# Optimization experiments

Hardware: AMD Instinct MI355X
Metric: run time of the kernel (lower is better)

The kernel has to match this reference:

```python
import jax, jax.numpy as jnp
import numpy as np

N = 50000   # nodes
E = 800000  # edges (avg degree 16)
G = 32      # graphs in batch
IN = 128; HID = 64; H = 2; C = 16
NEG_SLOPE = 0.2
BN_EPS = 1e-5


def setup_inputs() -> dict:
    key = jax.random.key(0)
    ks = jax.random.split(key, 16)
    def rn(k, shape, scale=0.1):
        return jax.random.normal(k, shape, jnp.float32) * scale
    return {
        "feat": jax.random.normal(ks[0], (N, IN), jnp.float32),
        "W0": rn(ks[1], (IN, H * HID)),
        "attn0": rn(ks[2], (H, HID)),
        "W1": rn(ks[3], (H * HID, H * HID)),
        "attn1": rn(ks[4], (H, HID)),
        "W2": rn(ks[5], (H * HID, H * HID)),
        "attn2": rn(ks[6], (H, HID)),
        "Wf": rn(ks[7], (H * HID, H * C)),
        "attnf": rn(ks[8], (H, C)),
        "mlp_w1": rn(ks[9], (C, C)),
        "mlp_gamma": jnp.ones((C,), jnp.float32),
        "mlp_beta": jnp.zeros((C,), jnp.float32),
        "mlp_w2": rn(ks[10], (C, C)),
        "src": jax.random.randint(ks[11], (E,), 0, N, jnp.int32),
        "dst": jax.random.randint(ks[12], (E,), 0, N, jnp.int32),
        "node_graph": jnp.sort(jax.random.randint(ks[13], (N,), 0, G, jnp.int32)),
        "num_graphs": G,
    }


def gatv2_layer(h, src, dst, W, attn, act):
    """DGL GATv2Conv with share_weights=True, bias=False, residual=False."""
    n = h.shape[0]
    nh, d = attn.shape
    z = (h @ W).reshape(n, nh, d)                      # [N,H,D]
    zs = z[src]                                        # [E,H,D] gather (src)
    e = jax.nn.leaky_relu(zs + z[dst], NEG_SLOPE)      # [E,H,D]
    score = jnp.einsum('ehd,hd->eh', e, attn)          # [E,H]
    # edge softmax over incoming edges of dst (shift-invariant max trick)
    m = jax.lax.stop_gradient(jax.ops.segment_max(score, dst, num_segments=n))
    a = jnp.exp(score - m[dst])
    denom = jax.ops.segment_sum(a, dst, num_segments=n)[dst]
    alpha = a / jnp.where(denom == 0, 1.0, denom)      # [E,H]
    out = jax.ops.segment_sum(alpha[..., None] * zs, dst, num_segments=n)  # [N,H,D]
    return act(out) if act is not None else out


def reference(feat, W0, attn0, W1, attn1, W2, attn2, Wf, attnf,
              mlp_w1, mlp_gamma, mlp_beta, mlp_w2,
              src, dst, node_graph, num_graphs):
    relu = jax.nn.relu
    n = feat.shape[0]
    h = gatv2_layer(feat, src, dst, W0, attn0, relu).reshape(n, -1)
    h = gatv2_layer(h, src, dst, W1, attn1, relu).reshape(n, -1)
    h = gatv2_layer(h, src, dst, W2, attn2, relu).reshape(n, -1)
    logits = gatv2_layer(h, src, dst, Wf, attnf, None).mean(axis=1)  # [N,C]
    pooled = jax.ops.segment_sum(logits, node_graph, num_segments=num_graphs)  # [G,C]
    # MLP: relu(batchnorm(lin0(x))) -> lin1 (training-mode batch stats, biased var)
    h1 = pooled @ mlp_w1
    mu = h1.mean(axis=0)
    var = h1.var(axis=0)
    h1 = (h1 - mu) / jnp.sqrt(var + BN_EPS) * mlp_gamma + mlp_beta
    out = relu(h1) @ mlp_w2
    return jax.nn.log_softmax(out, axis=-1)
```

## Files before the change

kernel.cpp:

```cpp
#include <hip/hip_runtime.h>
#include <hip/hip_bf16.h>
#include <hip/hip_fp16.h>
#include <math.h>

#define NN 50000
#define EE 800000
#define GG 32
#define HD 64
#define NHEAD 2
#define CCLS 16
#define NEG_SLOPE 0.2f
#define BN_EPS 1e-5f
#define LOG2E 1.4426950408889634f
#define STRIDE 64

typedef unsigned int u32;
typedef _Float16 hv2 __attribute__((ext_vector_type(2)));
typedef __fp16   cv2 __attribute__((ext_vector_type(2)));

__device__ __forceinline__ hv2 bch2(u32 u) { union { u32 u; hv2 h; } c; c.u = u; return c.h; }
__device__ __forceinline__ u32 pkrtz(float a, float b) {
    cv2 r = __builtin_amdgcn_cvt_pkrtz(a, b);
    union { cv2 h; u32 u; } c; c.h = r; return c.u;
}
__device__ __forceinline__ hv2 h2max(hv2 a, hv2 b) {
    return __builtin_elementwise_max(a, b);
}
__device__ __forceinline__ float fdot2(hv2 a, hv2 b, float c) {
#if __has_builtin(__builtin_amdgcn_fdot2)
    union { hv2 h; cv2 c2; } ua, ub;
    ua.h = a; ub.h = b;
    return __builtin_amdgcn_fdot2(ua.c2, ub.c2, c, false);
#else
    return fmaf((float)a[0], (float)b[0], fmaf((float)a[1], (float)b[1], c));
#endif
}


__global__ __launch_bounds__(256) void init_kernel(int* cursor, float* pooled) {
    int t = blockIdx.x * 256 + threadIdx.x;
    if (t < NN) cursor[t] = t * STRIDE;
    if (t < GG * CCLS) pooled[t] = 0.f;
}

__global__ __launch_bounds__(256) void scatter_kernel(const int* __restrict__ src,
                                                      const int* __restrict__ dst,
                                                      int* __restrict__ cursor,
                                                      int* __restrict__ csr_src) {
    int e = blockIdx.x * 256 + threadIdx.x;
    if (e < EE) {
        int p = atomicAdd(&cursor[dst[e]], 1);
        __builtin_nontemporal_store(src[e], &csr_src[p]);
    }
}


template<int KOUT, int RPT, bool F16IN>
__global__ __launch_bounds__(256) void gemm_kernel(const void* __restrict__ hv,
                                                   const float* __restrict__ W,
                                                   u32* __restrict__ z, int n) {
    constexpr int CG = KOUT / 4;
    constexpr int RT = 256 / CG;
    constexpr int BR = RT * RPT;
    constexpr int KB = 64;
    constexpr int HSTR = 132;
    __shared__ __align__(16) float Ws[KB * KOUT];
    __shared__ __align__(16) float hs[BR * HSTR];
    int t = threadIdx.x;
    int row0 = blockIdx.x * BR;

    if (F16IN) {
        const uint4* h = (const uint4*)hv;
        for (int i = t; i < BR * 16; i += 256) {
            int r = i >> 4, c8 = i & 15;
            int gr = row0 + r;
            uint4 u = {0, 0, 0, 0};
            if (gr < n) u = h[(size_t)gr * 16 + c8];
            hv2 p0 = bch2(u.x), p1 = bch2(u.y), p2 = bch2(u.z), p3 = bch2(u.w);
            float* d = &hs[r * HSTR + c8 * 8];
            d[0] = (float)p0[0]; d[1] = (float)p0[1];
            d[2] = (float)p1[0]; d[3] = (float)p1[1];
            d[4] = (float)p2[0]; d[5] = (float)p2[1];
            d[6] = (float)p3[0]; d[7] = (float)p3[1];
        }
    } else {
        const float4* h = (const float4*)hv;
        for (int i = t; i < BR * 32; i += 256) {
            int r = i >> 5, c4 = i & 31;
            int gr = row0 + r;
            float4 v = {0.f, 0.f, 0.f, 0.f};
            if (gr < n) v = h[(size_t)gr * 32 + c4];
            *(float4*)&hs[r * HSTR + c4 * 4] = v;
        }
    }

    int tc = t % CG, tr = t / CG;
    float4 acc[RPT];
    #pragma unroll
    for (int i = 0; i < RPT; i++) acc[i] = {0.f, 0.f, 0.f, 0.f};

    for (int kb = 0; kb < 128; kb += KB) {
        __syncthreads();
        for (int i = t; i < KB * CG; i += 256)
            ((float4*)Ws)[i] = ((const float4*)W)[kb * CG + i];
        __syncthreads();
        #pragma unroll 4
        for (int k = 0; k < KB; k += 4) {
            float4 w0 = ((float4*)Ws)[(k + 0) * CG + tc];
            float4 w1 = ((float4*)Ws)[(k + 1) * CG + tc];
            float4 w2 = ((float4*)Ws)[(k + 2) * CG + tc];
            float4 w3 = ((float4*)Ws)[(k + 3) * CG + tc];
            #pragma unroll
            for (int i = 0; i < RPT; i++) {
                float4 a4 = *(const float4*)&hs[(tr * RPT + i) * HSTR + kb + k];
                acc[i].x += a4.x * w0.x + a4.y * w1.x + a4.z * w2.x + a4.w * w3.x;
                acc[i].y += a4.x * w0.y + a4.y * w1.y + a4.z * w2.y + a4.w * w3.y;
                acc[i].z += a4.x * w0.z + a4.y * w1.z + a4.z * w2.z + a4.w * w3.z;
                acc[i].w += a4.x * w0.w + a4.y * w1.w + a4.z * w2.w + a4.w * w3.w;
            }
        }
    }
    for (int i = 0; i < RPT; i++) {
        int gr = row0 + tr * RPT + i;
        if (gr < n) {
            uint2 p;
            p.x = pkrtz(acc[i].x, acc[i].y);
            p.y = pkrtz(acc[i].z, acc[i].w);
            ((uint2*)z)[(size_t)gr * (KOUT / 4) + tc] = p;
        }
    }
}


__global__ __launch_bounds__(256) void edge_kernel(const u32* __restrict__ z,
                                                   const float* __restrict__ attn,
                                                   const int* __restrict__ cursor,
                                                   const int* __restrict__ csr_src,
                                                   u32* __restrict__ out, int n) {
    int wave = blockIdx.x * 4 + (threadIdx.x >> 6);
    int lane = threadIdx.x & 63;
    if (wave >= n) return;
    int i = wave;
    int slot = lane >> 3;
    int q8 = lane & 7;
    const uint4* zr = (const uint4*)z;

    size_t rowi = (size_t)i * 16 + q8 * 2;
    uint4 zua = zr[rowi], zub = zr[rowi + 1];
    hv2 zd[8] = {bch2(zua.x), bch2(zua.y), bch2(zua.z), bch2(zua.w),
                 bch2(zub.x), bch2(zub.y), bch2(zub.z), bch2(zub.w)};
    const float4* af = (const float4*)attn;
    float4 a0 = af[q8 * 4 + 0], a1 = af[q8 * 4 + 1];
    float4 a2 = af[q8 * 4 + 2], a3 = af[q8 * 4 + 3];
    hv2 ah[8] = {bch2(pkrtz(a0.x * LOG2E, a0.y * LOG2E)),
                 bch2(pkrtz(a0.z * LOG2E, a0.w * LOG2E)),
                 bch2(pkrtz(a1.x * LOG2E, a1.y * LOG2E)),
                 bch2(pkrtz(a1.z * LOG2E, a1.w * LOG2E)),
                 bch2(pkrtz(a2.x * LOG2E, a2.y * LOG2E)),
                 bch2(pkrtz(a2.z * LOG2E, a2.w * LOG2E)),
                 bch2(pkrtz(a3.x * LOG2E, a3.y * LOG2E)),
                 bch2(pkrtz(a3.z * LOG2E, a3.w * LOG2E))};
    const hv2 slope2 = {(_Float16)NEG_SLOPE, (_Float16)NEG_SLOPE};

    int base = i * STRIDE;
    int deg = cursor[i] - base;
    const int* ep = csr_src + base;

    float s = 0.f;
    float accf[16];
    #pragma unroll
    for (int j = 0; j < 16; j++) accf[j] = 0.f;

    for (int k = 0; k < deg; k += 8) {
        int kk = k + slot;
        bool valid = kk < deg;
        int sid = valid ? ep[kk] : i;
        size_t rs = (size_t)sid * 16 + q8 * 2;
        uint4 sa = zr[rs], sb = zr[rs + 1];
        hv2 zs[8] = {bch2(sa.x), bch2(sa.y), bch2(sa.z), bch2(sa.w),
                     bch2(sb.x), bch2(sb.y), bch2(sb.z), bch2(sb.w)};
        float sc = 0.f;
        #pragma unroll
        for (int j = 0; j < 8; j++) {
            hv2 x = zs[j] + zd[j];
            x = h2max(x, x * slope2);
            sc = fdot2(x, ah[j], sc);
        }
        sc += __shfl_xor(sc, 2, 64);
        sc += __shfl_xor(sc, 1, 64);
        float p = valid ? exp2f(sc) : 0.f;
        s += p;
        #pragma unroll
        for (int j = 0; j < 8; j++) {
            accf[2 * j]     = fmaf(p, (float)zs[j][0], accf[2 * j]);
            accf[2 * j + 1] = fmaf(p, (float)zs[j][1], accf[2 * j + 1]);
        }
    }

    #pragma unroll
    for (int off = 8; off <= 32; off <<= 1) {
        s += __shfl_xor(s, off, 64);
        #pragma unroll
        for (int j = 0; j < 16; j++) accf[j] += __shfl_xor(accf[j], off, 64);
    }

    if (slot == 0) {
        float inv = s > 0.f ? 1.f / s : 0.f;
        float o[16];
        #pragma unroll
        for (int j = 0; j < 16; j++) o[j] = fmaxf(accf[j] * inv, 0.f);
        uint4 pa, pb;
        pa.x = pkrtz(o[0], o[1]);   pa.y = pkrtz(o[2], o[3]);
        pa.z = pkrtz(o[4], o[5]);   pa.w = pkrtz(o[6], o[7]);
        pb.x = pkrtz(o[8], o[9]);   pb.y = pkrtz(o[10], o[11]);
        pb.z = pkrtz(o[12], o[13]); pb.w = pkrtz(o[14], o[15]);
        ((uint4*)out)[rowi] = pa;
        ((uint4*)out)[rowi + 1] = pb;
    }
}


__global__ __launch_bounds__(256) void edge_final_kernel(const u32* __restrict__ z,
                                                         const float* __restrict__ attn,
                                                         const int* __restrict__ cursor,
                                                         const int* __restrict__ csr_src,
                                                         float* __restrict__ logits, int n) {
    int wave = blockIdx.x * 4 + (threadIdx.x >> 6);
    int lane = threadIdx.x & 63;
    int iv = wave * 2 + (lane >> 5);
    bool mine = iv < n;
    int i = mine ? iv : (n - 1);
    int hl = lane & 31;
    int j = hl >> 3;
    int d8 = hl & 7;
    const uint2* zr = (const uint2*)z;
    uint2 zu = zr[(size_t)i * 8 + d8];
    hv2 zd0 = bch2(zu.x), zd1 = bch2(zu.y);
    float4 av = ((const float4*)attn)[d8];
    hv2 ah0 = bch2(pkrtz(av.x * LOG2E, av.y * LOG2E));
    hv2 ah1 = bch2(pkrtz(av.z * LOG2E, av.w * LOG2E));
    const hv2 slope2 = {(_Float16)NEG_SLOPE, (_Float16)NEG_SLOPE};
    int base = i * STRIDE;
    int deg = cursor[i] - base;
    const int* ep = csr_src + base;

    float s = 0.f;
    float accf[4] = {0.f, 0.f, 0.f, 0.f};
    for (int k = 0; k < deg; k += 4) {
        int kk = k + j;
        bool valid = kk < deg;
        int sid = valid ? ep[kk] : i;
        uint2 su = zr[(size_t)sid * 8 + d8];
        hv2 zs0 = bch2(su.x), zs1 = bch2(su.y);
        hv2 x;
        float sc = 0.f;
        x = zs0 + zd0; x = h2max(x, x * slope2); sc = fdot2(x, ah0, sc);
        x = zs1 + zd1; x = h2max(x, x * slope2); sc = fdot2(x, ah1, sc);
        sc += __shfl_xor(sc, 1, 64);
        sc += __shfl_xor(sc, 2, 64);
        float p = valid ? exp2f(sc) : 0.f;
        s += p;
        accf[0] = fmaf(p, (float)zs0[0], accf[0]);
        accf[1] = fmaf(p, (float)zs0[1], accf[1]);
        accf[2] = fmaf(p, (float)zs1[0], accf[2]);
        accf[3] = fmaf(p, (float)zs1[1], accf[3]);
    }
    #pragma unroll
    for (int off = 8; off <= 16; off <<= 1) {
        s += __shfl_xor(s, off, 64);
        #pragma unroll
        for (int jj = 0; jj < 4; jj++) accf[jj] += __shfl_xor(accf[jj], off, 64);
    }
    float inv = s > 0.f ? 1.f / s : 0.f;
    float4 o;
    o.x = accf[0] * inv; o.y = accf[1] * inv; o.z = accf[2] * inv; o.w = accf[3] * inv;
    o.x = 0.5f * (o.x + __shfl_xor(o.x, 4, 64));
    o.y = 0.5f * (o.y + __shfl_xor(o.y, 4, 64));
    o.z = 0.5f * (o.z + __shfl_xor(o.z, 4, 64));
    o.w = 0.5f * (o.w + __shfl_xor(o.w, 4, 64));
    if (mine && j == 0 && (hl & 4) == 0)
        ((float4*)logits)[i * 4 + (hl & 3)] = o;
}


__global__ __launch_bounds__(256) void pool_kernel(const float* __restrict__ logits,
                                                   const int* __restrict__ node_graph,
                                                   float* __restrict__ pooled) {
    int t = threadIdx.x;
    int c = t & 15;
    int ci = t >> 4;
    int start = blockIdx.x * 1024 + ci * 64;
    float acc = 0.f;
    int gcur = -1;
    for (int j = 0; j < 64; j++) {
        int node = start + j;
        if (node >= NN) break;
        int g = node_graph[node];
        if (g != gcur) {
            if (gcur >= 0) atomicAdd(&pooled[gcur * 16 + c], acc);
            gcur = g; acc = 0.f;
        }
        acc += logits[node * 16 + c];
    }
    if (gcur >= 0) atomicAdd(&pooled[gcur * 16 + c], acc);
}


__global__ __launch_bounds__(512) void mlp_kernel(const float* __restrict__ pooled,
                                                  const float* __restrict__ w1,
                                                  const float* __restrict__ gamma,
                                                  const float* __restrict__ beta,
                                                  const float* __restrict__ w2,
                                                  float* __restrict__ out) {
    __shared__ float P[GG * CCLS], H1[GG * CCLS], H2[GG * CCLS], O[GG * CCLS];
    __shared__ float mu[CCLS], rstd[CCLS], rowm[GG], rowl[GG];
    int t = threadIdx.x;
    int r = t >> 4, c = t & 15;
    if (t < GG * CCLS) P[t] = pooled[t];
    __syncthreads();
    if (t < GG * CCLS) {
        float s = 0.f;
        for (int k = 0; k < 16; k++) s += P[r * 16 + k] * w1[k * 16 + c];
        H1[t] = s;
    }
    __syncthreads();
    if (t < CCLS) {
        float s = 0.f;
        for (int rr = 0; rr < GG; rr++) s += H1[rr * 16 + t];
        float mn = s / GG;
        float s2 = 0.f;
        for (int rr = 0; rr < GG; rr++) { float d = H1[rr * 16 + t] - mn; s2 += d * d; }
        mu[t] = mn; rstd[t] = rsqrtf(s2 / GG + BN_EPS);
    }
    __syncthreads();
    if (t < GG * CCLS) {
        float v = (H1[t] - mu[c]) * rstd[c] * gamma[c] + beta[c];
        H2[t] = fmaxf(v, 0.f);
    }
    __syncthreads();
    if (t < GG * CCLS) {
        float s = 0.f;
        for (int k = 0; k < 16; k++) s += H2[r * 16 + k] * w2[k * 16 + c];
        O[t] = s;
    }
    __syncthreads();
    if (t < GG) {
        float mx = -INFINITY;
        for (int k = 0; k < 16; k++) mx = fmaxf(mx, O[t * 16 + k]);
        float l = 0.f;
        for (int k = 0; k < 16; k++) l += __expf(O[t * 16 + k] - mx);
        rowm[t] = mx; rowl[t] = logf(l);
    }
    __syncthreads();
    if (t < GG * CCLS) out[t] = O[t] - rowm[r] - rowl[r];
}


extern "C" void kernel_launch(void* const* d_in, const int* in_sizes, int n_in,
                              void* d_out, int out_size, void* d_ws, size_t ws_size,
                              hipStream_t stream) {
    const float* feat     = (const float*)d_in[0];
    const float* W0       = (const float*)d_in[1];
    const float* attn0    = (const float*)d_in[2];
    const float* W1       = (const float*)d_in[3];
    const float* attn1    = (const float*)d_in[4];
    const float* W2       = (const float*)d_in[5];
    const float* attn2    = (const float*)d_in[6];
    const float* Wf       = (const float*)d_in[7];
    const float* attnf    = (const float*)d_in[8];
    const float* mlp_w1   = (const float*)d_in[9];
    const float* mlp_g    = (const float*)d_in[10];
    const float* mlp_b    = (const float*)d_in[11];
    const float* mlp_w2   = (const float*)d_in[12];
    const int*   src      = (const int*)d_in[13];
    const int*   dst      = (const int*)d_in[14];
    const int*   ngraph   = (const int*)d_in[15];
    float* out = (float*)d_out;

    char* ws = (char*)d_ws;
    size_t off = 0;
    auto alloc = [&](size_t bytes) {
        void* p = ws + off;
        off = (off + bytes + 255) & ~(size_t)255;
        return p;
    };
    u32* z      = (u32*)alloc((size_t)NN * 64 * sizeof(u32));
    u32* hb0    = (u32*)alloc((size_t)NN * 64 * sizeof(u32));
    u32* hb1    = (u32*)alloc((size_t)NN * 64 * sizeof(u32));
    float* logits = (float*)alloc((size_t)NN * 16 * sizeof(float));
    float* pooled = (float*)alloc(GG * CCLS * sizeof(float));
    int* cursor   = (int*)alloc(NN * sizeof(int));
    int* csr_src  = (int*)alloc((size_t)NN * STRIDE * sizeof(int));

    init_kernel<<<(NN + 255) / 256, 256, 0, stream>>>(cursor, pooled);
    scatter_kernel<<<(EE + 255) / 256, 256, 0, stream>>>(src, dst, cursor, csr_src);

    int gemm_grid = (NN + 31) / 32;
    int edge_grid = (NN + 3) / 4;
    int edgef_grid = (NN + 7) / 8;

    gemm_kernel<128, 4, false><<<gemm_grid, 256, 0, stream>>>(feat, W0, z, NN);
    edge_kernel<<<edge_grid, 256, 0, stream>>>(z, attn0, cursor, csr_src, hb0, NN);

    gemm_kernel<128, 4, true><<<gemm_grid, 256, 0, stream>>>(hb0, W1, z, NN);
    edge_kernel<<<edge_grid, 256, 0, stream>>>(z, attn1, cursor, csr_src, hb1, NN);

    gemm_kernel<128, 4, true><<<gemm_grid, 256, 0, stream>>>(hb1, W2, z, NN);
    edge_kernel<<<edge_grid, 256, 0, stream>>>(z, attn2, cursor, csr_src, hb0, NN);

    gemm_kernel<32, 1, true><<<gemm_grid, 256, 0, stream>>>(hb0, Wf, z, NN);
    edge_final_kernel<<<edgef_grid, 256, 0, stream>>>(z, attnf, cursor, csr_src, logits, NN);

    pool_kernel<<<(NN + 1023) / 1024, 256, 0, stream>>>(logits, ngraph, pooled);
    mlp_kernel<<<1, 512, 0, stream>>>(pooled, mlp_w1, mlp_g, mlp_b, mlp_w2, out);
}
```

Baseline: 455.5 us.

## Rewrite GEMM with packed fp16 dot2 and fuse layer-0 GEMM with edge scatter

The GEMM now converts W and inputs to packed fp16 in shared memory and accumulates with fdot2, each thread producing 8 output columns. The whole weight matrix is loaded once instead of in two K-blocks, which removes one pair of barriers. The first-layer GEMM and the CSR scatter are merged into one launch using block-range dispatch, and the init kernel is replaced by memsets with a zero-based cursor. This cuts launch count and fp32 FMA work, at the cost of fp16 rounding of the layer-0 input features and weights.

After: 427.2 us. 6.2% less time.

```diff
diff --git a/kernel.cpp b/kernel.cpp
--- a/kernel.cpp
+++ b/kernel.cpp
@@ -37,96 +37,119 @@
 }
 
 
-__global__ __launch_bounds__(256) void init_kernel(int* cursor, float* pooled) {
-    int t = blockIdx.x * 256 + threadIdx.x;
-    if (t < NN) cursor[t] = t * STRIDE;
-    if (t < GG * CCLS) pooled[t] = 0.f;
-}
-
-__global__ __launch_bounds__(256) void scatter_kernel(const int* __restrict__ src,
-                                                      const int* __restrict__ dst,
-                                                      int* __restrict__ cursor,
-                                                      int* __restrict__ csr_src) {
-    int e = blockIdx.x * 256 + threadIdx.x;
-    if (e < EE) {
-        int p = atomicAdd(&cursor[dst[e]], 1);
-        __builtin_nontemporal_store(src[e], &csr_src[p]);
-    }
-}
-
+template<int KOUT, int RPT, bool F16IN>
+__device__ __forceinline__ void gemm_body(const void* __restrict__ hv,
+                                          const float* __restrict__ W,
+                                          u32* __restrict__ z, int n, int blk) {
+    constexpr int CT = KOUT / 8;
+    constexpr int RT = 256 / CT;
+    constexpr int BR = RT * RPT;
+    constexpr int WSTR = KOUT + 4;
+    __shared__ __align__(16) u32 WpD[64 * WSTR];
+    __shared__ __align__(16) uint4 hsU4[BR * 17];
+    int t = threadIdx.x;
+    int row0 = blk * BR;
+
+    for (int i = t; i < 64 * (KOUT / 4); i += 256) {
+        int k2 = i / (KOUT / 4), cq = i % (KOUT / 4);
+        float4 wa = ((const float4*)W)[(2 * k2) * (KOUT / 4) + cq];
+        float4 wb = ((const float4*)W)[(2 * k2 + 1) * (KOUT / 4) + cq];
+        uint4 d;
+        d.x = pkrtz(wa.x, wb.x); d.y = pkrtz(wa.y, wb.y);
+        d.z = pkrtz(wa.z, wb.z); d.w = pkrtz(wa.w, wb.w);
+        ((uint4*)&WpD[k2 * WSTR])[cq] = d;
+    }
+    for (int i = t; i < BR * 16; i += 256) {
+        int r = i >> 4, c16 = i & 15;
+        int gr = row0 + r;
+        uint4 u = {0, 0, 0, 0};
+        if (gr < n) {
+            if (F16IN) {
+                u = ((const uint4*)hv)[(size_t)gr * 16 + c16];
+            } else {
+                float4 f0 = ((const float4*)hv)[(size_t)gr * 32 + 2 * c16];
+                float4 f1 = ((const float4*)hv)[(size_t)gr * 32 + 2 * c16 + 1];
+                u.x = pkrtz(f0.x, f0.y); u.y = pkrtz(f0.z, f0.w);
+                u.z = pkrtz(f1.x, f1.y); u.w = pkrtz(f1.z, f1.w);
+            }
+        }
+        hsU4[r * 17 + c16] = u;
+    }
+    __syncthreads();
+
+    int tc = t % CT, tr = t / CT;
+    float acc[RPT][8];
+    #pragma unroll
+    for (int i = 0; i < RPT; i++)
+        #pragma unroll
+        for (int c = 0; c < 8; c++) acc[i][c] = 0.f;
+
+    for (int kq = 0; kq < 16; kq++) {
+        uint4 a4[RPT];
+        #pragma unroll
+        for (int i = 0; i < RPT; i++) a4[i] = hsU4[(tr * RPT + i) * 17 + kq];
+        #pragma unroll
+        for (int j = 0; j < 4; j++) {
+            const u32* wrow = &WpD[(4 * kq + j) * WSTR + tc * 8];
+            uint4 wa = *(const uint4*)wrow;
+            uint4 wb = *(const uint4*)(wrow + 4);
+            u32 wd[8] = {wa.x, wa.y, wa.z, wa.w, wb.x, wb.y, wb.z, wb.w};
+            #pragma unroll
+            for (int i = 0; i < RPT; i++) {
+                u32 av[4] = {a4[i].x, a4[i].y, a4[i].z, a4[i].w};
+                hv2 a2 = bch2(av[j]);
+                #pragma unroll
+                for (int c = 0; c < 8; c++)
+                    acc[i][c] = fdot2(a2, bch2(wd[c]), acc[i][c]);
+            }
+        }
+    }
+    #pragma unroll
+    for (int i = 0; i < RPT; i++) {
+        int gr = row0 + tr * RPT + i;
+        if (gr < n) {
+            uint4 p;
+            p.x = pkrtz(acc[i][0], acc[i][1]);
+            p.y = pkrtz(acc[i][2], acc[i][3]);
+            p.z = pkrtz(acc[i][4], acc[i][5]);
+            p.w = pkrtz(acc[i][6], acc[i][7]);
+            ((uint4*)z)[(size_t)gr * (KOUT / 8) + tc] = p;
+        }
+    }
+}
 
 template<int KOUT, int RPT, bool F16IN>
 __global__ __launch_bounds__(256) void gemm_kernel(const void* __restrict__ hv,
                                                    const float* __restrict__ W,
                                                    u32* __restrict__ z, int n) {
-    constexpr int CG = KOUT / 4;
-    constexpr int RT = 256 / CG;
-    constexpr int BR = RT * RPT;
-    constexpr int KB = 64;
-    constexpr int HSTR = 132;
-    __shared__ __align__(16) float Ws[KB * KOUT];
-    __shared__ __align__(16) float hs[BR * HSTR];
-    int t = threadIdx.x;
-    int row0 = blockIdx.x * BR;
-
-    if (F16IN) {
-        const uint4* h = (const uint4*)hv;
-        for (int i = t; i < BR * 16; i += 256) {
-            int r = i >> 4, c8 = i & 15;
-            int gr = row0 + r;
-            uint4 u = {0, 0, 0, 0};
-            if (gr < n) u = h[(size_t)gr * 16 + c8];
-            hv2 p0 = bch2(u.x), p1 = bch2(u.y), p2 = bch2(u.z), p3 = bch2(u.w);
-            float* d = &hs[r * HSTR + c8 * 8];
-            d[0] = (float)p0[0]; d[1] = (float)p0[1];
-            d[2] = (float)p1[0]; d[3] = (float)p1[1];
-            d[4] = (float)p2[0]; d[5] = (float)p2[1];
-            d[6] = (float)p3[0]; d[7] = (float)p3[1];
-        }
+    gemm_body<KOUT, RPT, F16IN>(hv, W, z, n, blockIdx.x);
+}
+
+
+#define GB0 782
+#define SB0 782
+
+__global__ __launch_bounds__(256) void gemm0_scatter_kernel(const float* __restrict__ feat,
+                                                            const float* __restrict__ W,
+                                                            u32* __restrict__ z,
+                                                            const int* __restrict__ src,
+                                                            const int* __restrict__ dst,
+                                                            int* __restrict__ cursor,
+                                                            int* __restrict__ csr_src) {
+    if (blockIdx.x < GB0) {
+        gemm_body<128, 4, false>(feat, W, z, NN, blockIdx.x);
     } else {
-        const float4* h = (const float4*)hv;
-        for (int i = t; i < BR * 32; i += 256) {
-            int r = i >> 5, c4 = i & 31;
-            int gr = row0 + r;
-            float4 v = {0.f, 0.f, 0.f, 0.f};
-            if (gr < n) v = h[(size_t)gr * 32 + c4];
-            *(float4*)&hs[r * HSTR + c4 * 4] = v;
-        }
-    }
-
-    int tc = t % CG, tr = t / CG;
-    float4 acc[RPT];
-    #pragma unroll
-    for (int i = 0; i < RPT; i++) acc[i] = {0.f, 0.f, 0.f, 0.f};
-
-    for (int kb = 0; kb < 128; kb += KB) {
-        __syncthreads();
-        for (int i = t; i < KB * CG; i += 256)
-            ((float4*)Ws)[i] = ((const float4*)W)[kb * CG + i];
-        __syncthreads();
-        #pragma unroll 4
-        for (int k = 0; k < KB; k += 4) {
-            float4 w0 = ((float4*)Ws)[(k + 0) * CG + tc];
-            float4 w1 = ((float4*)Ws)[(k + 1) * CG + tc];
-            float4 w2 = ((float4*)Ws)[(k + 2) * CG + tc];
-            float4 w3 = ((float4*)Ws)[(k + 3) * CG + tc];
-            #pragma unroll
-            for (int i = 0; i < RPT; i++) {
-                float4 a4 = *(const float4*)&hs[(tr * RPT + i) * HSTR + kb + k];
-                acc[i].x += a4.x * w0.x + a4.y * w1.x + a4.z * w2.x + a4.w * w3.x;
-                acc[i].y += a4.x * w0.y + a4.y * w1.y + a4.z * w2.y + a4.w * w3.y;
-                acc[i].z += a4.x * w0.z + a4.y * w1.z + a4.z * w2.z + a4.w * w3.z;
-                acc[i].w += a4.x * w0.w + a4.y * w1.w + a4.z * w2.w + a4.w * w3.w;
+        int b = blockIdx.x - GB0;
+        int e0 = b * 1024 + threadIdx.x;
+        #pragma unroll
+        for (int q = 0; q < 4; q++) {
+            int e = e0 + q * 256;
+            if (e < EE) {
+                int d = dst[e];
+                int s = src[e];
+                int p = atomicAdd(&cursor[d], 1);
+                csr_src[d * STRIDE + p] = s;
             }
-        }
-    }
-    for (int i = 0; i < RPT; i++) {
-        int gr = row0 + tr * RPT + i;
-        if (gr < n) {
-            uint2 p;
-            p.x = pkrtz(acc[i].x, acc[i].y);
-            p.y = pkrtz(acc[i].z, acc[i].w);
-            ((uint2*)z)[(size_t)gr * (KOUT / 4) + tc] = p;
         }
     }
 }
@@ -162,9 +185,8 @@
                  bch2(pkrtz(a3.z * LOG2E, a3.w * LOG2E))};
     const hv2 slope2 = {(_Float16)NEG_SLOPE, (_Float16)NEG_SLOPE};
 
-    int base = i * STRIDE;
-    int deg = cursor[i] - base;
-    const int* ep = csr_src + base;
+    int deg = cursor[i];
+    const int* ep = csr_src + i * STRIDE;
 
     float s = 0.f;
     float accf[16];
@@ -240,9 +262,8 @@
     hv2 ah0 = bch2(pkrtz(av.x * LOG2E, av.y * LOG2E));
     hv2 ah1 = bch2(pkrtz(av.z * LOG2E, av.w * LOG2E));
     const hv2 slope2 = {(_Float16)NEG_SLOPE, (_Float16)NEG_SLOPE};
-    int base = i * STRIDE;
-    int deg = cursor[i] - base;
-    const int* ep = csr_src + base;
+    int deg = cursor[i];
+    const int* ep = csr_src + i * STRIDE;
 
     float s = 0.f;
     float accf[4] = {0.f, 0.f, 0.f, 0.f};
@@ -392,14 +413,15 @@
     int* cursor   = (int*)alloc(NN * sizeof(int));
     int* csr_src  = (int*)alloc((size_t)NN * STRIDE * sizeof(int));
 
-    init_kernel<<<(NN + 255) / 256, 256, 0, stream>>>(cursor, pooled);
-    scatter_kernel<<<(EE + 255) / 256, 256, 0, stream>>>(src, dst, cursor, csr_src);
-
-    int gemm_grid = (NN + 31) / 32;
+    hipMemsetAsync(cursor, 0, NN * sizeof(int), stream);
+    hipMemsetAsync(pooled, 0, GG * CCLS * sizeof(float), stream);
+
     int edge_grid = (NN + 3) / 4;
     int edgef_grid = (NN + 7) / 8;
-
-    gemm_kernel<128, 4, false><<<gemm_grid, 256, 0, stream>>>(feat, W0, z, NN);
+    int gemm_grid = (NN + 63) / 64;
+
+    gemm0_scatter_kernel<<<GB0 + SB0, 256, 0, stream>>>(feat, W0, z, src, dst,
+                                                        cursor, csr_src);
     edge_kernel<<<edge_grid, 256, 0, stream>>>(z, attn0, cursor, csr_src, hb0, NN);
 
     gemm_kernel<128, 4, true><<<gemm_grid, 256, 0, stream>>>(hb0, W1, z, NN);
```
